# Performance work log

Hardware: AMD Instinct MI355X
Metric: run time of the kernel (lower is better)

Reference implementation:

```python
import jax, jax.numpy as jnp
import numpy as np

B, L, D, NH, V, T, CYC = 16, 512, 512, 8, 8000, 17, 2
HD = D // NH


def _attn(q, kv, qw, qb, kw, kb, vw, vb, ow, ob):
    # q: [N, Lq, D], kv: [N, Lk, D]; weights stored [in, out] (= torch W.T)
    N, Lq, _ = q.shape
    Lk = kv.shape[1]
    Q = (q @ qw + qb).reshape(N, Lq, NH, HD)
    K = (kv @ kw + kb).reshape(N, Lk, NH, HD)
    Vv = (kv @ vw + vb).reshape(N, Lk, NH, HD)
    scores = jnp.einsum('nqhd,nkhd->nhqk', Q, K) / np.float32(np.sqrt(HD))
    probs = jax.nn.softmax(scores, axis=-1)
    ctx = jnp.einsum('nhqk,nkhd->nqhd', probs, Vv).reshape(N, Lq, D)
    return ctx @ ow + ob


def _ln(x, w, b, eps=1e-12):
    u = x.mean(-1, keepdims=True)
    s = ((x - u) ** 2).mean(-1, keepdims=True)
    return w * (x - u) / jnp.sqrt(s + eps) + b


def setup_inputs() -> dict:
    key = jax.random.key(0)
    ks = jax.random.split(key, 32)
    p = {}
    p['tokens'] = jax.random.randint(ks[0], (B, L, 1), 0, V)
    p['masks'] = jnp.ones((B, L), dtype=jnp.int64)
    p['heads'] = jax.random.randint(ks[1], (B, L), 0, 2)
    p['tails'] = jax.random.randint(ks[2], (B, L), 0, 2)
    p['char_emb'] = jax.random.normal(ks[3], (V, D), jnp.float32) * 0.02
    i = 4
    for pre in ('sat', 'rel'):
        for nm in ('q', 'k', 'v', 'o'):
            p[f'{pre}_{nm}w'] = jax.random.normal(ks[i], (D, D), jnp.float32) * 0.02
            p[f'{pre}_{nm}b'] = jnp.zeros((D,), jnp.float32)
            i += 1
    p['ln_sat_w'] = jnp.ones((D,), jnp.float32)
    p['ln_sat_b'] = jnp.zeros((D,), jnp.float32)
    p['ln_rel_w'] = jnp.ones((D,), jnp.float32)
    p['ln_rel_b'] = jnp.zeros((D,), jnp.float32)
    p['ofc_w'] = jax.random.normal(ks[i], (D, T), jnp.float32) * 0.02
    p['ofc_b'] = jnp.zeros((T,), jnp.float32)
    return p


def reference(tokens, masks, heads, tails, char_emb,
              sat_qw, sat_qb, sat_kw, sat_kb, sat_vw, sat_vb, sat_ow, sat_ob,
              rel_qw, rel_qb, rel_kw, rel_kb, rel_vw, rel_vb, rel_ow, rel_ob,
              ln_sat_w, ln_sat_b, ln_rel_w, ln_rel_b, ofc_w, ofc_b):
    e = char_emb[tokens[:, :, 0]]  # [B, L, D]
    h = e
    s = e.mean(axis=1)  # relay token [B, D] (avg_pool2d over seq)
    for _ in range(CYC):
        # backward cycle_shift in the source is a correct roll-by-(-1)
        h_last = jnp.roll(h, -1, axis=1)
        # forward cycle_shift in the source is sequential in-place: result[:,0]=h[:,-1],
        # result[:,i>=1]=h[:,0] (the write at i=0 propagates). Reproduced faithfully.
        h_next = jnp.concatenate(
            [h[:, -1:, :], jnp.broadcast_to(h[:, :1, :], (B, L - 1, D))], axis=1)
        sm = jnp.broadcast_to(s[:, None, :], (B, L, D))
        c = jnp.stack([h_last, h, h_next, e, sm], axis=2).reshape(B * L, 5, D)
        hq = h.reshape(B * L, 1, D)
        a = _attn(hq, c, sat_qw, sat_qb, sat_kw, sat_kb, sat_vw, sat_vb, sat_ow, sat_ob)
        h = _ln(jax.nn.relu(a), ln_sat_w, ln_sat_b).reshape(B, L, D)
        mc = jnp.concatenate([s[:, None, :], h], axis=1)  # [B, L+1, D]
        r = _attn(s[:, None, :], mc, rel_qw, rel_qb, rel_kw, rel_kb, rel_vw, rel_vb, rel_ow, rel_ob)
        s = _ln(jax.nn.relu(r), ln_rel_w, ln_rel_b)[:, 0, :]
    logits = h @ ofc_w + ofc_b  # [B, L, T]
    return logits
```

## Files before the change

kernel.cpp:

```cpp
#include <hip/hip_runtime.h>
#include <hip/hip_bf16.h>

typedef __hip_bfloat16 bf16;

#define BB 16
#define LL 512
#define DD 512
#define NHH 8
#define HDD 64
#define TT 17
#define MM (BB*LL)
#define RCH 8
#define RCK 65

typedef __attribute__((ext_vector_type(8))) short bfrag;
typedef __attribute__((ext_vector_type(4))) float ffrag;
typedef __attribute__((ext_vector_type(8))) unsigned short us8;

static __device__ __forceinline__ void gld16(const void* g, void* l){
  __builtin_amdgcn_global_load_lds((const __attribute__((address_space(1))) void*)g,
                                   (__attribute__((address_space(3))) void*)l, 16, 0, 0);
}
static __device__ __forceinline__ float us2f(unsigned short u){
  unsigned int v = ((unsigned int)u) << 16;
  float f; __builtin_memcpy(&f, &v, 4); return f;
}

__global__ __launch_bounds__(256)
void emean(const int* __restrict__ tokens, const float* __restrict__ emb,
           bf16* __restrict__ ebf, float* __restrict__ mpart){
  int blk = blockIdx.x;
  int b = blk >> 4, lc = blk & 15;
  int t = threadIdx.x;
  __shared__ int toks[32];
  if (t < 32) toks[t] = tokens[b*LL + lc*32 + t];
  __syncthreads();
  bf16* eb = ebf + ((size_t)b*LL + lc*32)*DD;
  for (int d = t; d < DD; d += 256){
    float acc = 0.f;
    #pragma unroll 4
    for (int l = 0; l < 32; l++){
      float v = emb[(size_t)toks[l]*DD + d];
      eb[(size_t)l*DD + d] = __float2bfloat16(v);
      acc += v;
    }
    mpart[(size_t)blk*DD + d] = acc;
  }
}
__global__ void mean2(const float* __restrict__ part, float* __restrict__ s){
  int i = blockIdx.x*256 + threadIdx.x;
  int b = i >> 9, d = i & 511;
  float acc = 0.f;
  #pragma unroll
  for (int c = 0; c < 16; c++) acc += part[(size_t)(b*16 + c)*DD + d];
  s[i] = acc * (1.0f/LL);
}

__global__ void prep_w(const float* __restrict__ i0, const float* __restrict__ i1,
                       const float* __restrict__ i2, const float* __restrict__ i3,
                       const float* __restrict__ i4, const float* __restrict__ i5,
                       const float* __restrict__ wlog,
                       bf16* __restrict__ o0, bf16* __restrict__ o1,
                       bf16* __restrict__ o2, bf16* __restrict__ o3,
                       bf16* __restrict__ o4, bf16* __restrict__ o5,
                       bf16* __restrict__ olog){
  int z = blockIdx.z;
  int tx = threadIdx.x, ty = threadIdx.y;
  if (z == 6){
    int tid = ty*32 + tx;
    int i = ((blockIdx.y*16 + blockIdx.x) << 8) + tid;
    int row = i >> 9, k = i & 511;
    olog[i] = __float2bfloat16(row < TT ? wlog[(size_t)k*TT + row] : 0.f);
    return;
  }
  __shared__ float tile[32][33];
  const float* in = (z==0)?i0:(z==1)?i1:(z==2)?i2:(z==3)?i3:(z==4)?i4:i5;
  bf16* out       = (z==0)?o0:(z==1)?o1:(z==2)?o2:(z==3)?o3:(z==4)?o4:o5;
  int bx = blockIdx.x*32, by = blockIdx.y*32;
  #pragma unroll
  for (int j = 0; j < 32; j += 8)
    tile[ty + j][tx] = in[(size_t)(by + ty + j)*DD + bx + tx];
  __syncthreads();
  #pragma unroll
  for (int j = 0; j < 32; j += 8)
    out[(size_t)(bx + ty + j)*DD + by + tx] = __float2bfloat16(tile[tx][ty + j]);
}

__global__ __launch_bounds__(256)
void gemm_mfma_bf(const bf16* __restrict__ A, const bf16* __restrict__ Wt,
                  const float* __restrict__ b0, const float* __restrict__ b1,
                  const float* __restrict__ b2, const float* __restrict__ b3,
                  const float* __restrict__ b4,
                  bf16* __restrict__ D0, int ld0,
                  bf16* __restrict__ D1, int ld1, int split){
  const int K = 512;
  __shared__ bf16 As[128*32];
  __shared__ bf16 Bs[128*32];
  int t = threadIdx.x;
  int wave = t >> 6, lane = t & 63;
  int bm = blockIdx.y * 128, bn = blockIdx.x * 128;
  int wm = (wave & 1) * 64, wn = (wave >> 1) * 64;
  ffrag acc[4][4];
  #pragma unroll
  for (int i = 0; i < 4; i++)
    #pragma unroll
    for (int j = 0; j < 4; j++) acc[i][j] = (ffrag){0.f,0.f,0.f,0.f};

  int srow = t >> 2;
  int scol = (t & 3) * 8;
  const bf16* gA = A  + (size_t)(bm + srow)*K + scol;
  const bf16* gB = Wt + (size_t)(bn + srow)*K + scol;
  char* lA = (char*)As + 16*t;
  char* lB = (char*)Bs + 16*t;
  int q = lane >> 4, r = lane & 15;

  for (int k0 = 0; k0 < K; k0 += 32){
    gld16(gA + k0,          lA);
    gld16(gA + 64*K + k0,   lA + 4096);
    gld16(gB + k0,          lB);
    gld16(gB + 64*K + k0,   lB + 4096);
    __syncthreads();
    bfrag af[4], bfv[4];
    #pragma unroll
    for (int i = 0; i < 4; i++){
      af[i]  = *(const bfrag*)(As + (wm + i*16 + r)*32 + q*8);
      bfv[i] = *(const bfrag*)(Bs + (wn + i*16 + r)*32 + q*8);
    }
    #pragma unroll
    for (int i = 0; i < 4; i++)
      #pragma unroll
      for (int j = 0; j < 4; j++)
        acc[i][j] = __builtin_amdgcn_mfma_f32_16x16x32_bf16(af[i], bfv[j], acc[i][j], 0, 0, 0);
    __syncthreads();
  }
  #pragma unroll
  for (int i = 0; i < 4; i++){
    #pragma unroll
    for (int j = 0; j < 4; j++){
      int row = bm + wm + i*16 + q*4;
      int col = bn + wn + j*16 + r;
      const float* bp = (col < 512) ? b0 : (col < 1024) ? b1 :
                        (col < 1536) ? b2 : (col < 2048) ? b3 : b4;
      float bias = bp[col & 511];
      bf16* D; int ld;
      if (col < split){ D = D0 + (size_t)row*ld0 + col;         ld = ld0; }
      else            { D = D1 + (size_t)row*ld1 + (col-split); ld = ld1; }
      #pragma unroll
      for (int g = 0; g < 4; g++)
        D[(size_t)g*ld] = __float2bfloat16(acc[i][j][g] + bias);
    }
  }
}

__global__ __launch_bounds__(256)
void gemm_logits(const bf16* __restrict__ A, const bf16* __restrict__ Wt,
                 const float* __restrict__ bias, float* __restrict__ C){
  const int K = 512;
  __shared__ bf16 As[128*32];
  __shared__ bf16 Bs[128*32];
  int t = threadIdx.x;
  int wave = t >> 6, lane = t & 63;
  int bm = blockIdx.y * 128;
  int wm = (wave & 1) * 64, wn = (wave >> 1) * 64;
  ffrag acc[4][4];
  #pragma unroll
  for (int i = 0; i < 4; i++)
    #pragma unroll
    for (int j = 0; j < 4; j++) acc[i][j] = (ffrag){0.f,0.f,0.f,0.f};

  int srow = t >> 2;
  int scol = (t & 3) * 8;
  const bf16* gA = A  + (size_t)(bm + srow)*K + scol;
  const bf16* gB = Wt + (size_t)srow*K + scol;
  char* lA = (char*)As + 16*t;
  char* lB = (char*)Bs + 16*t;
  int q = lane >> 4, r = lane & 15;

  for (int k0 = 0; k0 < K; k0 += 32){
    gld16(gA + k0,          lA);
    gld16(gA + 64*K + k0,   lA + 4096);
    gld16(gB + k0,          lB);
    gld16(gB + 64*K + k0,   lB + 4096);
    __syncthreads();
    bfrag af[4], bfv[4];
    #pragma unroll
    for (int i = 0; i < 4; i++){
      af[i]  = *(const bfrag*)(As + (wm + i*16 + r)*32 + q*8);
      bfv[i] = *(const bfrag*)(Bs + (wn + i*16 + r)*32 + q*8);
    }
    #pragma unroll
    for (int i = 0; i < 4; i++)
      #pragma unroll
      for (int j = 0; j < 4; j++)
        acc[i][j] = __builtin_amdgcn_mfma_f32_16x16x32_bf16(af[i], bfv[j], acc[i][j], 0, 0, 0);
    __syncthreads();
  }
  #pragma unroll
  for (int i = 0; i < 4; i++){
    #pragma unroll
    for (int j = 0; j < 4; j++){
      int row = bm + wm + i*16 + q*4;
      int col = wn + j*16 + r;
      if (col < TT){
        float bias_v = bias[col];
        #pragma unroll
        for (int g = 0; g < 4; g++)
          C[(size_t)(row + g)*TT + col] = acc[i][j][g] + bias_v;
      }
    }
  }
}

__global__ __launch_bounds__(256)
void s_proj(const float* __restrict__ A,
            const float* __restrict__ W0, const float* __restrict__ W1,
            const float* __restrict__ W2, const float* __restrict__ W3,
            const float* __restrict__ W4,
            const float* __restrict__ bias0, const float* __restrict__ bias1,
            const float* __restrict__ bias2, const float* __restrict__ bias3,
            const float* __restrict__ bias4,
            float* __restrict__ O0, float* __restrict__ O1,
            float* __restrict__ O2, float* __restrict__ O3,
            float* __restrict__ O4,
            int ldc0, int ldc1, int ldc2, int ldc3, int ldc4){
  __shared__ float part[8][32][17];
  int t = threadIdx.x;
  int n = t & 31, kg = t >> 5;
  int wi = blockIdx.x >> 4, ch = blockIdx.x & 15;
  const float* W  = (wi==0)?W0:(wi==1)?W1:(wi==2)?W2:(wi==3)?W3:W4;
  const float* bs = (wi==0)?bias0:(wi==1)?bias1:(wi==2)?bias2:(wi==3)?bias3:bias4;
  float* O  = (wi==0)?O0:(wi==1)?O1:(wi==2)?O2:(wi==3)?O3:O4;
  int ldc   = (wi==0)?ldc0:(wi==1)?ldc1:(wi==2)?ldc2:(wi==3)?ldc3:ldc4;
  int col = ch*32 + n;
  float acc[16];
  #pragma unroll
  for (int m = 0; m < 16; m++) acc[m] = 0.f;
  const float* Wp = W + (size_t)(kg*64)*512 + col;
  const float* Ap = A + kg*64;
  for (int k = 0; k < 64; k++){
    float w = Wp[(size_t)k*512];
    #pragma unroll
    for (int m = 0; m < 16; m++) acc[m] = fmaf(Ap[m*512 + k], w, acc[m]);
  }
  #pragma unroll
  for (int m = 0; m < 16; m++) part[kg][n][m] = acc[m];
  __syncthreads();
  for (int o = t; o < 512; o += 256){
    int m = o >> 5, nn = o & 31;
    float v = 0.f;
    #pragma unroll
    for (int g = 0; g < 8; g++) v += part[g][nn][m];
    O[(size_t)m*ldc + ch*32 + nn] = v + bs[ch*32 + nn];
  }
}

__global__ void sat_attn(const bf16* __restrict__ qp, int sq,
                         const bf16* __restrict__ kp, const bf16* __restrict__ vp, int skv,
                         const bf16* __restrict__ KeVe, const float* __restrict__ KsVs,
                         bf16* __restrict__ ctx){
  int gw = blockIdx.x*(blockDim.x >> 6) + (threadIdx.x >> 6);
  int lane = threadIdx.x & 63;
  int hh = gw & (NHH-1);
  int t  = gw >> 3;
  int b = t >> 9, l = t & 511;
  int base = hh*HDD + lane;
  float qv = __bfloat162float(qp[(size_t)t*sq + base]);
  int t0 = (b << 9) | ((l + 1) & 511);
  int t2 = (b << 9) | (l == 0 ? 511 : 0);
  float k[5];
  k[0] = __bfloat162float(kp  [(size_t)t0*skv + base]);
  k[1] = __bfloat162float(kp  [(size_t)t *skv + base]);
  k[2] = __bfloat162float(kp  [(size_t)t2*skv + base]);
  k[3] = __bfloat162float(KeVe[(size_t)t *1024 + base]);
  k[4] = KsVs[(size_t)b *1024 + base];
  float sc[5];
  #pragma unroll
  for (int j = 0; j < 5; j++){
    float v = qv * k[j];
    #pragma unroll
    for (int off = 32; off; off >>= 1) v += __shfl_xor(v, off, 64);
    sc[j] = v * 0.125f;
  }
  float m = fmaxf(fmaxf(fmaxf(sc[0],sc[1]), fmaxf(sc[2],sc[3])), sc[4]);
  float p[5], den = 0.f;
  #pragma unroll
  for (int j = 0; j < 5; j++){ p[j] = __expf(sc[j]-m); den += p[j]; }
  float inv = 1.0f/den;
  float v0 = __bfloat162float(vp  [(size_t)t0*skv + base]);
  float v1 = __bfloat162float(vp  [(size_t)t *skv + base]);
  float v2 = __bfloat162float(vp  [(size_t)t2*skv + base]);
  float v3 = __bfloat162float(KeVe[(size_t)t *1024 + 512 + base]);
  float v4 = KsVs[(size_t)b *1024 + 512 + base];
  float o = (p[0]*v0 + p[1]*v1 + p[2]*v2 + p[3]*v3 + p[4]*v4) * inv;
  ctx[(size_t)t*DD + base] = __float2bfloat16(o);
}

__global__ __launch_bounds__(256)
void rel_part(const float* __restrict__ q, const float* __restrict__ Ksr,
              const float* __restrict__ Vsr, const bf16* __restrict__ KV,
              float* __restrict__ pws){
  int ch = blockIdx.x, hh = blockIdx.y, b = blockIdx.z;
  int t = threadIdx.x;
  int base = hh * HDD;
  __shared__ __align__(16) float qs[64];
  __shared__ float sc[RCK];
  __shared__ float red[256];
  __shared__ float part[4][64];
  int j0 = ch * RCK;
  int nk = min(513 - j0, RCK);
  if (t < 64) qs[t] = q[(size_t)b*DD + base + t];
  __syncthreads();
  if (t < nk){
    int j = j0 + t;
    float a = 0.f;
    if (j == 0){
      const float* kr = Ksr + (size_t)b*DD + base;
      #pragma unroll
      for (int d = 0; d < 64; d += 4){
        float4 k4 = *(const float4*)(kr + d);
        float4 q4 = *(const float4*)(qs + d);
        a += q4.x*k4.x + q4.y*k4.y + q4.z*k4.z + q4.w*k4.w;
      }
    } else {
      const bf16* kr = KV + ((size_t)b*LL + j - 1)*1024 + base;
      #pragma unroll
      for (int d = 0; d < 64; d += 8){
        us8 k8 = *(const us8*)(kr + d);
        #pragma unroll
        for (int g = 0; g < 8; g++) a += qs[d+g] * us2f(k8[g]);
      }
    }
    sc[t] = a * 0.125f;
  }
  __syncthreads();
  red[t] = (t < nk) ? sc[t] : -1e30f; __syncthreads();
  for (int st = 128; st; st >>= 1){ if (t < st) red[t] = fmaxf(red[t], red[t+st]); __syncthreads(); }
  float m = red[0]; __syncthreads();
  if (t < nk) sc[t] = __expf(sc[t] - m);
  __syncthreads();
  red[t] = (t < nk) ? sc[t] : 0.f; __syncthreads();
  for (int st = 128; st; st >>= 1){ if (t < st) red[t] += red[t+st]; __syncthreads(); }
  float l = red[0];
  int d = t & 63, c2 = t >> 6;
  float a = 0.f;
  for (int j = c2; j < nk; j += 4){
    int gj = j0 + j;
    float vv = (gj == 0) ? Vsr[(size_t)b*DD + base + d]
                         : __bfloat162float(KV[((size_t)b*LL + gj - 1)*1024 + 512 + base + d]);
    a += sc[j] * vv;
  }
  part[c2][d] = a; __syncthreads();
  float* o = pws + (((size_t)(b*NHH + hh))*RCH + ch) * 66;
  if (t < 64) o[t] = part[0][t] + part[1][t] + part[2][t] + part[3][t];
  else if (t == 64) o[64] = m;
  else if (t == 65) o[65] = l;
}

__global__ __launch_bounds__(256)
void rel_tail(const float* __restrict__ pws, const float* __restrict__ W,
              const float* __restrict__ bias, const float* __restrict__ lnw,
              const float* __restrict__ lnb, float* __restrict__ s){
  int b = blockIdx.x;
  int t = threadIdx.x;
  __shared__ float crs[512];
  __shared__ float red[256];
  for (int o = t; o < 512; o += 256){
    int hh = o >> 6, d = o & 63;
    const float* p = pws + ((size_t)(b*NHH + hh))*RCH*66;
    float M = -1e30f;
    #pragma unroll
    for (int c = 0; c < RCH; c++) M = fmaxf(M, p[c*66 + 64]);
    float den = 0.f, acc = 0.f;
    #pragma unroll
    for (int c = 0; c < RCH; c++){
      float w = __expf(p[c*66 + 64] - M);
      den += w * p[c*66 + 65];
      acc += w * p[c*66 + d];
    }
    crs[o] = acc / den;
  }
  __syncthreads();
  int n0 = t, n1 = t + 256;
  float a0 = 0.f, a1 = 0.f;
  for (int k = 0; k < 512; k++){
    float c = crs[k];
    a0 = fmaf(c, W[(size_t)k*512 + n0], a0);
    a1 = fmaf(c, W[(size_t)k*512 + n1], a1);
  }
  a0 += bias[n0]; a1 += bias[n1];
  float v0 = fmaxf(a0, 0.f), v1 = fmaxf(a1, 0.f);
  red[t] = v0 + v1; __syncthreads();
  for (int st = 128; st; st >>= 1){ if (t < st) red[t] += red[t+st]; __syncthreads(); }
  float u = red[0] * (1.0f/DD); __syncthreads();
  float d0 = v0 - u, d1 = v1 - u;
  red[t] = d0*d0 + d1*d1; __syncthreads();
  for (int st = 128; st; st >>= 1){ if (t < st) red[t] += red[t+st]; __syncthreads(); }
  float inv = rsqrtf(red[0] * (1.0f/DD) + 1e-12f);
  s[(size_t)b*DD + n0] = lnw[n0]*d0*inv + lnb[n0];
  s[(size_t)b*DD + n1] = lnw[n1]*d1*inv + lnb[n1];
}

__global__ void relu_ln_bf(const bf16* __restrict__ X, const float* __restrict__ w,
                           const float* __restrict__ bn, bf16* __restrict__ Ybf){
  int row = blockIdx.x;
  int tid = threadIdx.x;
  __shared__ float red[256];
  const bf16* x = X + (size_t)row*DD;
  float v0 = fmaxf(__bfloat162float(x[tid]), 0.f);
  float v1 = fmaxf(__bfloat162float(x[tid+256]), 0.f);
  red[tid] = v0 + v1;
  __syncthreads();
  for (int st = 128; st; st >>= 1){ if (tid < st) red[tid] += red[tid+st]; __syncthreads(); }
  float u = red[0] * (1.0f/DD);
  __syncthreads();
  float d0 = v0 - u, d1 = v1 - u;
  red[tid] = d0*d0 + d1*d1;
  __syncthreads();
  for (int st = 128; st; st >>= 1){ if (tid < st) red[tid] += red[tid+st]; __syncthreads(); }
  float var = red[0] * (1.0f/DD);
  float inv = rsqrtf(var + 1e-12f);
  Ybf[(size_t)row*DD + tid]       = __float2bfloat16(w[tid]    *d0*inv + bn[tid]);
  Ybf[(size_t)row*DD + tid + 256] = __float2bfloat16(w[tid+256]*d1*inv + bn[tid+256]);
}

extern "C" void kernel_launch(void* const* d_in, const int* in_sizes, int n_in,
                              void* d_out, int out_size, void* d_ws, size_t ws_size,
                              hipStream_t stream) {
  const int*   tokens  = (const int*)  d_in[0];
  const float* emb     = (const float*)d_in[4];
  const float* sat_qw  = (const float*)d_in[5];
  const float* sat_qb  = (const float*)d_in[6];
  const float* sat_kw  = (const float*)d_in[7];
  const float* sat_kb  = (const float*)d_in[8];
  const float* sat_vw  = (const float*)d_in[9];
  const float* sat_vb  = (const float*)d_in[10];
  const float* sat_ow  = (const float*)d_in[11];
  const float* sat_ob  = (const float*)d_in[12];
  const float* rel_qw  = (const float*)d_in[13];
  const float* rel_qb  = (const float*)d_in[14];
  const float* rel_kw  = (const float*)d_in[15];
  const float* rel_kb  = (const float*)d_in[16];
  const float* rel_vw  = (const float*)d_in[17];
  const float* rel_vb  = (const float*)d_in[18];
  const float* rel_ow  = (const float*)d_in[19];
  const float* rel_ob  = (const float*)d_in[20];
  const float* ln_sat_w= (const float*)d_in[21];
  const float* ln_sat_b= (const float*)d_in[22];
  const float* ln_rel_w= (const float*)d_in[23];
  const float* ln_rel_b= (const float*)d_in[24];
  const float* ofc_w   = (const float*)d_in[25];
  const float* ofc_b   = (const float*)d_in[26];

  char* p = (char*)d_ws;
  auto alloc = [&](size_t bytes) -> char* {
    char* r = p; p += (bytes + 255) & ~(size_t)255; return r;
  };
  const size_t BIGH = (size_t)MM*DD*2;
  bf16*  ebf   = (bf16*) alloc(BIGH);
  bf16*  qkv   = (bf16*) alloc(3*BIGH);
  bf16*  kvbuf = (bf16*) alloc(2*BIGH);
  bf16*  KeVe  = (bf16*) alloc(2*BIGH);
  bf16*  qbuf  = (bf16*) alloc(BIGH);
  bf16*  ctxbf = (bf16*) alloc(BIGH);
  bf16*  WtAll = (bf16*) alloc((size_t)2560*512*2);
  bf16*  WtO   = (bf16*) alloc((size_t)512*512*2);
  bf16*  WtLog = (bf16*) alloc((size_t)128*512*2);
  float* s     = (float*)alloc(BB*DD*4);
  float* KsVs  = (float*)alloc(BB*1024*4);
  float* qr    = (float*)alloc(BB*DD*4);
  float* Ksr   = (float*)alloc(BB*DD*4);
  float* Vsr   = (float*)alloc(BB*DD*4);
  float* mpart = (float*)alloc((size_t)256*DD*4);
  float* pws   = (float*)alloc((size_t)BB*NHH*RCH*66*4);
  bf16*  hbf   = ebf;
  bf16*  aout  = qkv;

  emean<<<256, 256, 0, stream>>>(tokens, emb, ebf, mpart);
  mean2<<<32, 256, 0, stream>>>(mpart, s);

  prep_w<<<dim3(16,16,7), dim3(32,8), 0, stream>>>(
      sat_qw, sat_kw, sat_vw, rel_kw, rel_vw, sat_ow, ofc_w,
      WtAll, WtAll + (size_t)512*512, WtAll + (size_t)1024*512,
      WtAll + (size_t)1536*512, WtAll + (size_t)2048*512, WtO, WtLog);

  gemm_mfma_bf<<<dim3(12,64), 256, 0, stream>>>(ebf, WtAll,
      sat_qb, sat_kb, sat_vb, sat_vb, sat_vb, qbuf, 512, KeVe, 1024, 512);
  s_proj<<<80, 256, 0, stream>>>(s,
      sat_kw, sat_vw, rel_qw, rel_kw, rel_vw,
      sat_kb, sat_vb, rel_qb, rel_kb, rel_vb,
      KsVs, KsVs + 512, qr, Ksr, Vsr,
      1024, 1024, 512, 512, 512);
  sat_attn<<<MM*NHH/4, 256, 0, stream>>>(qbuf, 512, KeVe, KeVe + 512, 1024,
                                         KeVe, KsVs, ctxbf);
  gemm_mfma_bf<<<dim3(4,64), 256, 0, stream>>>(ctxbf, WtO,
      sat_ob, sat_ob, sat_ob, sat_ob, sat_ob, aout, 512, aout, 512, 512);
  relu_ln_bf<<<MM, 256, 0, stream>>>(aout, ln_sat_w, ln_sat_b, hbf);
  gemm_mfma_bf<<<dim3(20,64), 256, 0, stream>>>(hbf, WtAll,
      sat_qb, sat_kb, sat_vb, rel_kb, rel_vb, qkv, 1536, kvbuf, 1024, 1536);
  rel_part<<<dim3(RCH, NHH, BB), 256, 0, stream>>>(qr, Ksr, Vsr, kvbuf, pws);
  rel_tail<<<BB, 256, 0, stream>>>(pws, rel_ow, rel_ob, ln_rel_w, ln_rel_b, s);

  s_proj<<<32, 256, 0, stream>>>(s,
      sat_kw, sat_vw, sat_vw, sat_vw, sat_vw,
      sat_kb, sat_vb, sat_vb, sat_vb, sat_vb,
      KsVs, KsVs + 512, Ksr, Ksr, Ksr,
      1024, 1024, 512, 512, 512);
  sat_attn<<<MM*NHH/4, 256, 0, stream>>>(qkv, 1536, qkv + 512, qkv + 1024, 1536,
                                         KeVe, KsVs, ctxbf);
  gemm_mfma_bf<<<dim3(4,64), 256, 0, stream>>>(ctxbf, WtO,
      sat_ob, sat_ob, sat_ob, sat_ob, sat_ob, aout, 512, aout, 512, 512);
  relu_ln_bf<<<MM, 256, 0, stream>>>(aout, ln_sat_w, ln_sat_b, hbf);

  gemm_logits<<<dim3(1,64), 256, 0, stream>>>(hbf, WtLog, ofc_b, (float*)d_out);
}
```

Measured before the change: 376.9 us.

## Vectorize sat_attn per token, swizzle GEMM block order, trim logits GEMM

sat_attn now assigns one wave per token instead of one wave per (token, head). Each lane loads 8 contiguous bf16 values with 16-byte loads and reduces over 8 lanes, replacing scalar loads and full-wave shuffles. The GEMM grid becomes 1D with a swizzled row-block mapping so neighbouring blocks share weight tiles in cache. The logits GEMM computes only the two 16-column tiles that cover the 17 outputs, with the other waves idle. The old gemm_logits is left as a dead stub.

```diff
diff --git a/kernel.cpp b/kernel.cpp
--- a/kernel.cpp
+++ b/kernel.cpp
@@ -24,6 +24,12 @@
 static __device__ __forceinline__ float us2f(unsigned short u){
   unsigned int v = ((unsigned int)u) << 16;
   float f; __builtin_memcpy(&f, &v, 4); return f;
+}
+static __device__ __forceinline__ float hsum8(float v){
+  v += __shfl_xor(v, 1);
+  v += __shfl_xor(v, 2);
+  v += __shfl_xor(v, 4);
+  return v;
 }
 
 __global__ __launch_bounds__(256)
@@ -98,7 +104,9 @@
   __shared__ bf16 Bs[128*32];
   int t = threadIdx.x;
   int wave = t >> 6, lane = t & 63;
-  int bm = blockIdx.y * 128, bn = blockIdx.x * 128;
+  int id = blockIdx.x;
+  int bm = (((id & 7) << 3) | ((id >> 3) & 7)) * 128;
+  int bn = (id >> 6) * 128;
   int wm = (wave & 1) * 64, wn = (wave >> 1) * 64;
   ffrag acc[4][4];
   #pragma unroll
@@ -162,11 +170,9 @@
   int wave = t >> 6, lane = t & 63;
   int bm = blockIdx.y * 128;
   int wm = (wave & 1) * 64, wn = (wave >> 1) * 64;
-  ffrag acc[4][4];
-  #pragma unroll
-  for (int i = 0; i < 4; i++)
-    #pragma unroll
-    for (int j = 0; j < 4; j++) acc[i][j] = (ffrag){0.f,0.f,0.f,0.f};
+  ffrag acc[2];
+  acc[0] = (ffrag){0.f,0.f,0.f,0.f};
+  acc[1] = (ffrag){0.f,0.f,0.f,0.f};
 
   int srow = t >> 2;
   int scol = (t & 3) * 8;
@@ -182,30 +188,80 @@
     gld16(gB + k0,          lB);
     gld16(gB + 64*K + k0,   lB + 4096);
     __syncthreads();
-    bfrag af[4], bfv[4];
+    if (wn == 0){
+      #pragma unroll
+      for (int i = 0; i < 4; i++){
+        bfrag af = *(const bfrag*)(As + (wm + i*16 + r)*32 + q*8);
+        if (i < 2){
+          bfrag bfv = *(const bfrag*)(Bs + (i*16 + r)*32 + q*8);
+        }
+      }
+      bfrag bf0 = *(const bfrag*)(Bs + (0*16 + r)*32 + q*8);
+      bfrag bf1 = *(const bfrag*)(Bs + (1*16 + r)*32 + q*8);
+      #pragma unroll
+      for (int i = 0; i < 4; i++){
+        bfrag af = *(const bfrag*)(As + (wm + i*16 + r)*32 + q*8);
+        (void)af; (void)bf0; (void)bf1;
+      }
+    }
+    __syncthreads();
+  }
+  (void)acc; (void)bias; (void)C; (void)wn;
+}
+
+__global__ __launch_bounds__(256)
+void gemm_logits2(const bf16* __restrict__ A, const bf16* __restrict__ Wt,
+                  const float* __restrict__ bias, float* __restrict__ C){
+  const int K = 512;
+  __shared__ bf16 As[128*32];
+  __shared__ bf16 Bs[128*32];
+  int t = threadIdx.x;
+  int wave = t >> 6, lane = t & 63;
+  int bm = blockIdx.y * 128;
+  int wm = (wave & 1) * 64, wn = (wave >> 1) * 64;
+  ffrag acc[4][2];
+  #pragma unroll
+  for (int i = 0; i < 4; i++){ acc[i][0] = (ffrag){0,0,0,0}; acc[i][1] = (ffrag){0,0,0,0}; }
+
+  int srow = t >> 2;
+  int scol = (t & 3) * 8;
+  const bf16* gA = A  + (size_t)(bm + srow)*K + scol;
+  const bf16* gB = Wt + (size_t)srow*K + scol;
+  char* lA = (char*)As + 16*t;
+  char* lB = (char*)Bs + 16*t;
+  int q = lane >> 4, r = lane & 15;
+
+  for (int k0 = 0; k0 < K; k0 += 32){
+    gld16(gA + k0,          lA);
+    gld16(gA + 64*K + k0,   lA + 4096);
+    gld16(gB + k0,          lB);
+    gld16(gB + 64*K + k0,   lB + 4096);
+    __syncthreads();
+    if (wn == 0){
+      bfrag bf0 = *(const bfrag*)(Bs + (r)*32 + q*8);
+      bfrag bf1 = *(const bfrag*)(Bs + (16 + r)*32 + q*8);
+      #pragma unroll
+      for (int i = 0; i < 4; i++){
+        bfrag af = *(const bfrag*)(As + (wm + i*16 + r)*32 + q*8);
+        acc[i][0] = __builtin_amdgcn_mfma_f32_16x16x32_bf16(af, bf0, acc[i][0], 0, 0, 0);
+        acc[i][1] = __builtin_amdgcn_mfma_f32_16x16x32_bf16(af, bf1, acc[i][1], 0, 0, 0);
+      }
+    }
+    __syncthreads();
+  }
+  if (wn == 0){
     #pragma unroll
     for (int i = 0; i < 4; i++){
-      af[i]  = *(const bfrag*)(As + (wm + i*16 + r)*32 + q*8);
-      bfv[i] = *(const bfrag*)(Bs + (wn + i*16 + r)*32 + q*8);
-    }
-    #pragma unroll
-    for (int i = 0; i < 4; i++)
-      #pragma unroll
-      for (int j = 0; j < 4; j++)
-        acc[i][j] = __builtin_amdgcn_mfma_f32_16x16x32_bf16(af[i], bfv[j], acc[i][j], 0, 0, 0);
-    __syncthreads();
-  }
-  #pragma unroll
-  for (int i = 0; i < 4; i++){
-    #pragma unroll
-    for (int j = 0; j < 4; j++){
-      int row = bm + wm + i*16 + q*4;
-      int col = wn + j*16 + r;
-      if (col < TT){
-        float bias_v = bias[col];
-        #pragma unroll
-        for (int g = 0; g < 4; g++)
-          C[(size_t)(row + g)*TT + col] = acc[i][j][g] + bias_v;
+      #pragma unroll
+      for (int j = 0; j < 2; j++){
+        int row = bm + wm + i*16 + q*4;
+        int col = j*16 + r;
+        if (col < TT){
+          float bias_v = bias[col];
+          #pragma unroll
+          for (int g = 0; g < 4; g++)
+            C[(size_t)(row + g)*TT + col] = acc[i][j][g] + bias_v;
+        }
       }
     }
   }
@@ -254,45 +310,71 @@
   }
 }
 
-__global__ void sat_attn(const bf16* __restrict__ qp, int sq,
-                         const bf16* __restrict__ kp, const bf16* __restrict__ vp, int skv,
-                         const bf16* __restrict__ KeVe, const float* __restrict__ KsVs,
-                         bf16* __restrict__ ctx){
-  int gw = blockIdx.x*(blockDim.x >> 6) + (threadIdx.x >> 6);
-  int lane = threadIdx.x & 63;
-  int hh = gw & (NHH-1);
-  int t  = gw >> 3;
-  int b = t >> 9, l = t & 511;
-  int base = hh*HDD + lane;
-  float qv = __bfloat162float(qp[(size_t)t*sq + base]);
-  int t0 = (b << 9) | ((l + 1) & 511);
-  int t2 = (b << 9) | (l == 0 ? 511 : 0);
-  float k[5];
-  k[0] = __bfloat162float(kp  [(size_t)t0*skv + base]);
-  k[1] = __bfloat162float(kp  [(size_t)t *skv + base]);
-  k[2] = __bfloat162float(kp  [(size_t)t2*skv + base]);
-  k[3] = __bfloat162float(KeVe[(size_t)t *1024 + base]);
-  k[4] = KsVs[(size_t)b *1024 + base];
+__global__ __launch_bounds__(256)
+void sat_attn(const bf16* __restrict__ qp, int sq,
+              const bf16* __restrict__ kp, const bf16* __restrict__ vp, int skv,
+              const bf16* __restrict__ KeVe, const float* __restrict__ KsVs,
+              bf16* __restrict__ ctx){
+  int tok = blockIdx.x*4 + (threadIdx.x >> 6);
+  int l = threadIdx.x & 63;
+  int b = tok >> 9, li = tok & 511;
+  int off = l*8;
+  int t0 = (b << 9) | ((li + 1) & 511);
+  int t2 = (b << 9) | (li == 0 ? 511 : 0);
+
+  float qf[8];
+  { us8 q8 = *(const us8*)(qp + (size_t)tok*sq + off);
+    #pragma unroll
+    for (int g = 0; g < 8; g++) qf[g] = us2f(q8[g]); }
+
   float sc[5];
-  #pragma unroll
-  for (int j = 0; j < 5; j++){
-    float v = qv * k[j];
-    #pragma unroll
-    for (int off = 32; off; off >>= 1) v += __shfl_xor(v, off, 64);
-    sc[j] = v * 0.125f;
-  }
+  int rows[3] = {t0, tok, t2};
+  #pragma unroll
+  for (int j = 0; j < 3; j++){
+    us8 k8 = *(const us8*)(kp + (size_t)rows[j]*skv + off);
+    float a = 0.f;
+    #pragma unroll
+    for (int g = 0; g < 8; g++) a += qf[g]*us2f(k8[g]);
+    sc[j] = hsum8(a) * 0.125f;
+  }
+  { us8 k8 = *(const us8*)(KeVe + (size_t)tok*1024 + off);
+    float a = 0.f;
+    #pragma unroll
+    for (int g = 0; g < 8; g++) a += qf[g]*us2f(k8[g]);
+    sc[3] = hsum8(a) * 0.125f; }
+  { const float* ks = KsVs + (size_t)b*1024 + off;
+    float4 f0 = *(const float4*)ks, f1 = *(const float4*)(ks + 4);
+    float a = qf[0]*f0.x + qf[1]*f0.y + qf[2]*f0.z + qf[3]*f0.w
+            + qf[4]*f1.x + qf[5]*f1.y + qf[6]*f1.z + qf[7]*f1.w;
+    sc[4] = hsum8(a) * 0.125f; }
+
   float m = fmaxf(fmaxf(fmaxf(sc[0],sc[1]), fmaxf(sc[2],sc[3])), sc[4]);
   float p[5], den = 0.f;
   #pragma unroll
   for (int j = 0; j < 5; j++){ p[j] = __expf(sc[j]-m); den += p[j]; }
   float inv = 1.0f/den;
-  float v0 = __bfloat162float(vp  [(size_t)t0*skv + base]);
-  float v1 = __bfloat162float(vp  [(size_t)t *skv + base]);
-  float v2 = __bfloat162float(vp  [(size_t)t2*skv + base]);
-  float v3 = __bfloat162float(KeVe[(size_t)t *1024 + 512 + base]);
-  float v4 = KsVs[(size_t)b *1024 + 512 + base];
-  float o = (p[0]*v0 + p[1]*v1 + p[2]*v2 + p[3]*v3 + p[4]*v4) * inv;
-  ctx[(size_t)t*DD + base] = __float2bfloat16(o);
+
+  float o[8];
+  #pragma unroll
+  for (int g = 0; g < 8; g++) o[g] = 0.f;
+  #pragma unroll
+  for (int j = 0; j < 3; j++){
+    us8 v8 = *(const us8*)(vp + (size_t)rows[j]*skv + off);
+    #pragma unroll
+    for (int g = 0; g < 8; g++) o[g] += p[j]*us2f(v8[g]);
+  }
+  { us8 v8 = *(const us8*)(KeVe + (size_t)tok*1024 + 512 + off);
+    #pragma unroll
+    for (int g = 0; g < 8; g++) o[g] += p[3]*us2f(v8[g]); }
+  { const float* vs = KsVs + (size_t)b*1024 + 512 + off;
+    float4 f0 = *(const float4*)vs, f1 = *(const float4*)(vs + 4);
+    o[0] += p[4]*f0.x; o[1] += p[4]*f0.y; o[2] += p[4]*f0.z; o[3] += p[4]*f0.w;
+    o[4] += p[4]*f1.x; o[5] += p[4]*f1.y; o[6] += p[4]*f1.z; o[7] += p[4]*f1.w; }
+
+  bf16 ob[8];
+  #pragma unroll
+  for (int g = 0; g < 8; g++) ob[g] = __float2bfloat16(o[g]*inv);
+  *(us8*)(ctx + (size_t)tok*DD + off) = *(const us8*)ob;
 }
 
 __global__ __launch_bounds__(256)
@@ -483,19 +565,19 @@
       WtAll, WtAll + (size_t)512*512, WtAll + (size_t)1024*512,
       WtAll + (size_t)1536*512, WtAll + (size_t)2048*512, WtO, WtLog);
 
-  gemm_mfma_bf<<<dim3(12,64), 256, 0, stream>>>(ebf, WtAll,
+  gemm_mfma_bf<<<12*64, 256, 0, stream>>>(ebf, WtAll,
       sat_qb, sat_kb, sat_vb, sat_vb, sat_vb, qbuf, 512, KeVe, 1024, 512);
   s_proj<<<80, 256, 0, stream>>>(s,
       sat_kw, sat_vw, rel_qw, rel_kw, rel_vw,
       sat_kb, sat_vb, rel_qb, rel_kb, rel_vb,
       KsVs, KsVs + 512, qr, Ksr, Vsr,
       1024, 1024, 512, 512, 512);
-  sat_attn<<<MM*NHH/4, 256, 0, stream>>>(qbuf, 512, KeVe, KeVe + 512, 1024,
-                                         KeVe, KsVs, ctxbf);
-  gemm_mfma_bf<<<dim3(4,64), 256, 0, stream>>>(ctxbf, WtO,
+  sat_attn<<<MM/4, 256, 0, stream>>>(qbuf, 512, KeVe, KeVe + 512, 1024,
+                                     KeVe, KsVs, ctxbf);
+  gemm_mfma_bf<<<4*64, 256, 0, stream>>>(ctxbf, WtO,
       sat_ob, sat_ob, sat_ob, sat_ob, sat_ob, aout, 512, aout, 512, 512);
   relu_ln_bf<<<MM, 256, 0, stream>>>(aout, ln_sat_w, ln_sat_b, hbf);
-  gemm_mfma_bf<<<dim3(20,64), 256, 0, stream>>>(hbf, WtAll,
+  gemm_mfma_bf<<<20*64, 256, 0, stream>>>(hbf, WtAll,
       sat_qb, sat_kb, sat_vb, rel_kb, rel_vb, qkv, 1536, kvbuf, 1024, 1536);
   rel_part<<<dim3(RCH, NHH, BB), 256, 0, stream>>>(qr, Ksr, Vsr, kvbuf, pws);
   rel_tail<<<BB, 256, 0, stream>>>(pws, rel_ow, rel_ob, ln_rel_w, ln_rel_b, s);
@@ -505,11 +587,11 @@
       sat_kb, sat_vb, sat_vb, sat_vb, sat_vb,
       KsVs, KsVs + 512, Ksr, Ksr, Ksr,
       1024, 1024, 512, 512, 512);
-  sat_attn<<<MM*NHH/4, 256, 0, stream>>>(qkv, 1536, qkv + 512, qkv + 1024, 1536,
-                                         KeVe, KsVs, ctxbf);
-  gemm_mfma_bf<<<dim3(4,64), 256, 0, stream>>>(ctxbf, WtO,
+  sat_attn<<<MM/4, 256, 0, stream>>>(qkv, 1536, qkv + 512, qkv + 1024, 1536,
+                                     KeVe, KsVs, ctxbf);
+  gemm_mfma_bf<<<4*64, 256, 0, stream>>>(ctxbf, WtO,
       sat_ob, sat_ob, sat_ob, sat_ob, sat_ob, aout, 512, aout, 512, 512);
   relu_ln_bf<<<MM, 256, 0, stream>>>(aout, ln_sat_w, ln_sat_b, hbf);
 
-  gemm_logits<<<dim3(1,64), 256, 0, stream>>>(hbf, WtLog, ofc_b, (float*)d_out);
-}
+  gemm_logits2<<<dim3(1,64), 256, 0, stream>>>(hbf, WtLog, ofc_b, (float*)d_out);
+}
```

Result: faster. 336.3 us (-10.8%).
